# Optimization experiments

Measured on AMD Instinct MI355X. Metric: run time of the kernel, lower is better.

Reference implementation:

```python
import jax, jax.numpy as jnp
import numpy as np

NUM_HEADS = 12

def setup_inputs() -> dict:
    key = jax.random.key(0)
    k1, k2, k3 = jax.random.split(key, 3)
    B, N, C = 8, 2048, 768
    x = jax.random.normal(k1, (B, N, C), dtype=jnp.float32)
    w_qkv = jax.random.normal(k2, (3 * C, C), dtype=jnp.float32) * (C ** -0.5)
    w_proj = jax.random.normal(k3, (C, C), dtype=jnp.float32) * (C ** -0.5)
    b_proj = jnp.zeros((C,), dtype=jnp.float32)
    return {"x": x, "w_qkv": w_qkv, "w_proj": w_proj, "b_proj": b_proj}

def reference(x, w_qkv, w_proj, b_proj):
    B, N, C = x.shape
    H = NUM_HEADS
    D = C // H
    scale = D ** -0.5
    # qkv: [B,N,3C] -> [3,B,H,N,D]
    qkv = (x @ w_qkv.T).reshape(B, N, 3, H, D).transpose(2, 0, 3, 1, 4)
    q, k, v = qkv[0], qkv[1], qkv[2]
    attn = jnp.einsum('bhnd,bhmd->bhnm', q, k) * scale  # [B,H,N,N]
    attn = jax.nn.softmax(attn, axis=-1)
    out = jnp.einsum('bhnm,bhmd->bhnd', attn, v)  # [B,H,N,D]
    out = out.transpose(0, 2, 1, 3).reshape(B, N, C)
    return out @ w_proj.T + b_proj
```

## Files before the change

kernel.cpp:

```cpp
#include <hip/hip_runtime.h>

typedef __bf16 bf16;
typedef __attribute__((ext_vector_type(8))) __bf16 bf16x8;
typedef __attribute__((ext_vector_type(4))) __bf16 bf16x4;
typedef __attribute__((ext_vector_type(4))) float f32x4;

#define NBATCH 8
#define NHEAD  12
#define SEQ    2048
#define DH     64
#define CDIM   768
#define MROWS  (NBATCH*SEQ)
#define NQKV   (3*CDIM)

__device__ __forceinline__ f32x4 mfma16(bf16x8 a, bf16x8 b, f32x4 c) {
  return __builtin_amdgcn_mfma_f32_16x16x32_bf16(a, b, c, 0, 0, 0);
}

__device__ __forceinline__ void gload_lds16(const void* g, void* l) {
  __builtin_amdgcn_global_load_lds((const __attribute__((address_space(1))) void*)g,
                                   (__attribute__((address_space(3))) void*)l,
                                   16, 0, 0);
}

__device__ __forceinline__ unsigned cvt_pk_bf16(float lo, float hi) {
  unsigned r;
  asm("v_cvt_pk_bf16_f32 %0, %1, %2" : "=v"(r) : "v"(lo), "v"(hi));
  return r;
}

__device__ __forceinline__ float exp2_raw(float x) {
  float r;
  asm("v_exp_f32 %0, %1" : "=v"(r) : "v"(x));
  return r;
}

__global__ void cvt_bf16(const float* __restrict__ src, bf16* __restrict__ dst, int n8) {
  int i = blockIdx.x * 256 + threadIdx.x;
  if (i >= n8) return;
  const float4* s4 = (const float4*)src;
  float4 a = s4[2*i], c = s4[2*i+1];
  bf16x8 o;
  o[0]=(bf16)a.x; o[1]=(bf16)a.y; o[2]=(bf16)a.z; o[3]=(bf16)a.w;
  o[4]=(bf16)c.x; o[5]=(bf16)c.y; o[6]=(bf16)c.z; o[7]=(bf16)c.w;
  *(bf16x8*)(dst + (size_t)i*8) = o;
}

template <int OUT_F32>
__global__ __launch_bounds__(256, 2)
void gemm_bt(const bf16* __restrict__ A, const bf16* __restrict__ Bm,
             void* __restrict__ Cout, const float* __restrict__ bias,
             int M, int Nn, int K) {
  __shared__ bf16 As[128*32];
  __shared__ bf16 Bs[128*32];
  const int tid = threadIdx.x, wid = tid >> 6, lane = tid & 63;
  const int g = lane >> 4, ln = lane & 15;
  const int ntn = Nn >> 7;
  const int gsz = 32 * ntn;
  const int grp = blockIdx.x / gsz;
  const int rem = blockIdx.x - grp * gsz;
  const int tm = grp * 32 + (rem & 31);
  const int tn = rem >> 5;
  const int m0 = tm << 7, n0 = tn << 7;
  const int wr = wid >> 1, wc = wid & 1;

  const int srow = lane >> 2;
  const int sslot = lane & 3;

  f32x4 acc[4][4] = {};

  const int nkt = K >> 5;
  for (int kt = 0; kt < nkt; ++kt) {
    if (kt) __syncthreads();
    #pragma unroll
    for (int i = 0; i < 2; ++i) {
      int c = wid * 2 + i;
      int row = c * 16 + srow;
      int colA = kt * 32 + ((sslot ^ (row & 3)) << 3);
      gload_lds16(A + (size_t)(m0 + row) * K + colA, &As[c * 512]);
      gload_lds16(Bm + (size_t)(n0 + row) * K + colA, &Bs[c * 512]);
    }
    __syncthreads();

    bf16x8 aF[4], bF[4];
    #pragma unroll
    for (int m = 0; m < 4; ++m) {
      int row = wr * 64 + m * 16 + ln;
      aF[m] = *(const bf16x8*)&As[row * 32 + ((g ^ (row & 3)) << 3)];
    }
    #pragma unroll
    for (int n = 0; n < 4; ++n) {
      int row = wc * 64 + n * 16 + ln;
      bF[n] = *(const bf16x8*)&Bs[row * 32 + ((g ^ (row & 3)) << 3)];
    }
    #pragma unroll
    for (int m = 0; m < 4; ++m)
      #pragma unroll
      for (int n = 0; n < 4; ++n)
        acc[m][n] = mfma16(aF[m], bF[n], acc[m][n]);
  }

  #pragma unroll
  for (int m = 0; m < 4; ++m) {
    int rowb = m0 + wr * 64 + m * 16 + g * 4;
    #pragma unroll
    for (int n = 0; n < 4; ++n) {
      int col = n0 + wc * 64 + n * 16 + ln;
      float bv = OUT_F32 ? bias[col] : 0.f;
      #pragma unroll
      for (int r = 0; r < 4; ++r) {
        if (OUT_F32)
          ((float*)Cout)[(size_t)(rowb + r) * Nn + col] = acc[m][n][r] + bv;
        else
          ((bf16*)Cout)[(size_t)(rowb + r) * Nn + col] = (bf16)acc[m][n][r];
      }
    }
  }
}

__global__ __launch_bounds__(256)
void split_v(const bf16* __restrict__ qkv, bf16* __restrict__ Vt) {
  __shared__ bf16 vlds[64 * 72];
  const int nt = blockIdx.x, bh = blockIdx.y;
  const int b = bh / NHEAD, h = bh % NHEAD;
  const int tid = threadIdx.x;
  const int nl = tid >> 2, quad = tid & 3;

  const bf16* s = qkv + ((size_t)(b * SEQ + nt * 64 + nl)) * NQKV + 2 * CDIM + h * DH + quad * 16;
  *(bf16x8*)&vlds[nl * 72 + quad * 16] = *(const bf16x8*)s;
  *(bf16x8*)&vlds[nl * 72 + quad * 16 + 8] = *(const bf16x8*)(s + 8);
  __syncthreads();
  const int dl = tid >> 2;
  bf16x8 w0, w1;
  #pragma unroll
  for (int j = 0; j < 8; ++j) {
    w0[j] = vlds[(quad * 16 + j) * 72 + dl];
    w1[j] = vlds[(quad * 16 + 8 + j) * 72 + dl];
  }
  bf16* d = Vt + ((size_t)bh * DH + dl) * SEQ + nt * 64 + quad * 16;
  *(bf16x8*)d = w0;
  *(bf16x8*)(d + 8) = w1;
}

__global__ __launch_bounds__(128, 2)
void attn_fwd8(const bf16* __restrict__ qkv, const bf16* __restrict__ Vt,
               bf16* __restrict__ Oa) {
  __shared__ bf16 Ks[2][64 * 64];
  __shared__ bf16 Vs[2][64 * 64];
  const int tid = threadIdx.x, wid = tid >> 6, lane = tid & 63;
  const int g = lane >> 4, ln = lane & 15;
  const int qt = blockIdx.x, bh = blockIdx.y;
  const int b = bh / NHEAD, h = bh % NHEAD;

  const bf16* QrowA = qkv + ((size_t)b * SEQ + qt * 64 + wid * 32 + ln) * NQKV + h * DH;
  const bf16* QrowB = QrowA + (size_t)16 * NQKV;
  const bf16x8 qA0 = *(const bf16x8*)(QrowA + g * 8);
  const bf16x8 qA1 = *(const bf16x8*)(QrowA + 32 + g * 8);
  const bf16x8 qB0 = *(const bf16x8*)(QrowB + g * 8);
  const bf16x8 qB1 = *(const bf16x8*)(QrowB + 32 + g * 8);

  const int sr = lane >> 3, sl = lane & 7;
  const bf16* kp[4];
  const bf16* vp[4];
  int lofs[4];
  #pragma unroll
  for (int i = 0; i < 4; ++i) {
    const int c = wid * 4 + i;
    const int pr = c * 8 + sr;
    const int sw = (sl ^ (pr & 7)) << 3;
    const int keyK = ((pr >> 5) & 1) * 32 + ((pr >> 4) & 1) * 4 + ((pr >> 2) & 3) * 8 + (pr & 3);
    kp[i] = qkv + ((size_t)b * SEQ + keyK) * NQKV + CDIM + h * DH + sw;
    vp[i] = Vt + ((size_t)bh * DH + pr) * SEQ + sw;
    lofs[i] = c * 512;
  }
  const size_t KADV = (size_t)64 * NQKV;

  const int e7 = ln & 7;
  const int off0 = ln * 64 + ((g ^ e7) << 3);
  const int off1 = ln * 64 + (((4 | g) ^ e7) << 3);

  const bf16 one = (bf16)1.0f;
  const bf16x8 onesF = {one, one, one, one, one, one, one, one};

  f32x4 oA[4] = {}, oB[4] = {};
  f32x4 laccA = {0.f, 0.f, 0.f, 0.f}, laccB = {0.f, 0.f, 0.f, 0.f};
  float mA = -3.0e38f, mB = -3.0e38f;
  const float SC = 0.125f * 1.44269504088896f;

  #pragma unroll
  for (int i = 0; i < 4; ++i) {
    gload_lds16(kp[i], &Ks[0][lofs[i]]);
    gload_lds16(vp[i], &Vs[0][lofs[i]]);
  }
  __syncthreads();

  int cur = 0;
  for (int t = 0; t < SEQ / 64; ++t) {
    if (t < SEQ / 64 - 1) {
      const int nb = cur ^ 1;
      #pragma unroll
      for (int i = 0; i < 4; ++i) {
        kp[i] += KADV; vp[i] += 64;
        gload_lds16(kp[i], &Ks[nb][lofs[i]]);
        gload_lds16(vp[i], &Vs[nb][lofs[i]]);
      }
    }
    const bf16* KsB = &Ks[cur][0];
    const bf16* VsB = &Vs[cur][0];

    f32x4 sA[4] = {}, sB[4] = {};
    #pragma unroll
    for (int nt = 0; nt < 4; ++nt) {
      bf16x8 kF0 = *(const bf16x8*)(KsB + off0 + nt * 1024);
      bf16x8 kF1 = *(const bf16x8*)(KsB + off1 + nt * 1024);
      sA[nt] = mfma16(kF0, qA0, sA[nt]);
      sA[nt] = mfma16(kF1, qA1, sA[nt]);
      sB[nt] = mfma16(kF0, qB0, sB[nt]);
      sB[nt] = mfma16(kF1, qB1, sB[nt]);
    }

    float a0 = fmaxf(fmaxf(sA[0][0], sA[0][1]), fmaxf(sA[0][2], sA[0][3]));
    float a1 = fmaxf(fmaxf(sA[1][0], sA[1][1]), fmaxf(sA[1][2], sA[1][3]));
    float a2 = fmaxf(fmaxf(sA[2][0], sA[2][1]), fmaxf(sA[2][2], sA[2][3]));
    float a3 = fmaxf(fmaxf(sA[3][0], sA[3][1]), fmaxf(sA[3][2], sA[3][3]));
    float rA = fmaxf(fmaxf(a0, a1), fmaxf(a2, a3));
    rA = fmaxf(rA, __shfl_xor(rA, 16, 64));
    rA = fmaxf(rA, __shfl_xor(rA, 32, 64));
    float b0 = fmaxf(fmaxf(sB[0][0], sB[0][1]), fmaxf(sB[0][2], sB[0][3]));
    float b1 = fmaxf(fmaxf(sB[1][0], sB[1][1]), fmaxf(sB[1][2], sB[1][3]));
    float b2 = fmaxf(fmaxf(sB[2][0], sB[2][1]), fmaxf(sB[2][2], sB[2][3]));
    float b3 = fmaxf(fmaxf(sB[3][0], sB[3][1]), fmaxf(sB[3][2], sB[3][3]));
    float rB = fmaxf(fmaxf(b0, b1), fmaxf(b2, b3));
    rB = fmaxf(rB, __shfl_xor(rB, 16, 64));
    rB = fmaxf(rB, __shfl_xor(rB, 32, 64));
    const float rsA = rA * SC, rsB = rB * SC;

    if (__any(rsA > mA + 8.0f || rsB > mB + 8.0f)) {
      float nmA = fmaxf(mA, rsA), nmB = fmaxf(mB, rsB);
      float alA = exp2_raw(mA - nmA), alB = exp2_raw(mB - nmB);
      mA = nmA; mB = nmB;
      float alrA[4], alrB[4];
      #pragma unroll
      for (int r = 0; r < 4; ++r) {
        alrA[r] = __shfl(alA, g * 4 + r, 64);
        alrB[r] = __shfl(alB, g * 4 + r, 64);
      }
      #pragma unroll
      for (int dt = 0; dt < 4; ++dt)
        #pragma unroll
        for (int r = 0; r < 4; ++r) { oA[dt][r] *= alrA[r]; oB[dt][r] *= alrB[r]; }
      #pragma unroll
      for (int r = 0; r < 4; ++r) { laccA[r] *= alrA[r]; laccB[r] *= alrB[r]; }
    }

    bf16x8 pA[2], pB[2];
    #pragma unroll
    for (int kk = 0; kk < 2; ++kk) {
      union { bf16x8 v; unsigned u[4]; } w;
      w.u[0] = cvt_pk_bf16(exp2_raw(fmaf(sA[2*kk][0], SC, -mA)),
                           exp2_raw(fmaf(sA[2*kk][1], SC, -mA)));
      w.u[1] = cvt_pk_bf16(exp2_raw(fmaf(sA[2*kk][2], SC, -mA)),
                           exp2_raw(fmaf(sA[2*kk][3], SC, -mA)));
      w.u[2] = cvt_pk_bf16(exp2_raw(fmaf(sA[2*kk+1][0], SC, -mA)),
                           exp2_raw(fmaf(sA[2*kk+1][1], SC, -mA)));
      w.u[3] = cvt_pk_bf16(exp2_raw(fmaf(sA[2*kk+1][2], SC, -mA)),
                           exp2_raw(fmaf(sA[2*kk+1][3], SC, -mA)));
      pA[kk] = w.v;
      w.u[0] = cvt_pk_bf16(exp2_raw(fmaf(sB[2*kk][0], SC, -mB)),
                           exp2_raw(fmaf(sB[2*kk][1], SC, -mB)));
      w.u[1] = cvt_pk_bf16(exp2_raw(fmaf(sB[2*kk][2], SC, -mB)),
                           exp2_raw(fmaf(sB[2*kk][3], SC, -mB)));
      w.u[2] = cvt_pk_bf16(exp2_raw(fmaf(sB[2*kk+1][0], SC, -mB)),
                           exp2_raw(fmaf(sB[2*kk+1][1], SC, -mB)));
      w.u[3] = cvt_pk_bf16(exp2_raw(fmaf(sB[2*kk+1][2], SC, -mB)),
                           exp2_raw(fmaf(sB[2*kk+1][3], SC, -mB)));
      pB[kk] = w.v;
    }

    #pragma unroll
    for (int kk = 0; kk < 2; ++kk) {
      laccA = mfma16(pA[kk], onesF, laccA);
      laccB = mfma16(pB[kk], onesF, laccB);
      const int voff = kk ? off1 : off0;
      #pragma unroll
      for (int dt = 0; dt < 4; ++dt) {
        bf16x8 vF = *(const bf16x8*)(VsB + voff + dt * 1024);
        oA[dt] = mfma16(pA[kk], vF, oA[dt]);
        oB[dt] = mfma16(pB[kk], vF, oB[dt]);
      }
    }
    __syncthreads();
    cur ^= 1;
  }

  float invA[4], invB[4];
  #pragma unroll
  for (int r = 0; r < 4; ++r) { invA[r] = 1.0f / laccA[r]; invB[r] = 1.0f / laccB[r]; }

  #pragma unroll
  for (int r = 0; r < 4; ++r) {
    bf16* OrA = Oa + ((size_t)b * SEQ + qt * 64 + wid * 32 + g * 4 + r) * CDIM + h * DH + ln;
    bf16* OrB = OrA + (size_t)16 * CDIM;
    #pragma unroll
    for (int dt = 0; dt < 4; ++dt) {
      OrA[dt * 16] = (bf16)(oA[dt][r] * invA[r]);
      OrB[dt * 16] = (bf16)(oB[dt][r] * invB[r]);
    }
  }
}

extern "C" void kernel_launch(void* const* d_in, const int* in_sizes, int n_in,
                              void* d_out, int out_size, void* d_ws, size_t ws_size,
                              hipStream_t stream) {
  const float* x      = (const float*)d_in[0];
  const float* w_qkv  = (const float*)d_in[1];
  const float* w_proj = (const float*)d_in[2];
  const float* b_proj = (const float*)d_in[3];

  char* ws = (char*)d_ws;
  bf16* x_bf    = (bf16*)(ws + 0);
  bf16* wqkv_bf = (bf16*)(ws + 25165824);
  bf16* wproj_bf= (bf16*)(ws + 28704768);
  bf16* qkv     = (bf16*)(ws + 29884416);
  bf16* attn_o  = (bf16*)(ws + 105381888);
  bf16* Vtb     = (bf16*)(ws + 130547712);

  cvt_bf16<<<dim3((MROWS*CDIM/8 + 255)/256), 256, 0, stream>>>(x, x_bf, MROWS*CDIM/8);
  cvt_bf16<<<dim3((NQKV*CDIM/8 + 255)/256), 256, 0, stream>>>(w_qkv, wqkv_bf, NQKV*CDIM/8);
  cvt_bf16<<<dim3((CDIM*CDIM/8 + 255)/256), 256, 0, stream>>>(w_proj, wproj_bf, CDIM*CDIM/8);

  gemm_bt<0><<<dim3((MROWS/128)*(NQKV/128)), 256, 0, stream>>>(
      x_bf, wqkv_bf, qkv, nullptr, MROWS, NQKV, CDIM);

  split_v<<<dim3(SEQ/64, NBATCH*NHEAD), 256, 0, stream>>>(qkv, Vtb);

  attn_fwd8<<<dim3(SEQ/64, NBATCH*NHEAD), 128, 0, stream>>>(qkv, Vtb, attn_o);

  gemm_bt<1><<<dim3((MROWS/128)*(CDIM/128)), 256, 0, stream>>>(
      attn_o, wproj_bf, (float*)d_out, b_proj, MROWS, CDIM, CDIM);
}
```

Before: 311.9 us.

## Triple-buffer K/V loads and overlap next-tile QK^T with current softmax

The attention kernel moves from double to triple buffering of K/V tiles in LDS, with explicit vmcnt waits replacing full barriers so two tiles stay in flight. It also software-pipelines the loop by computing the QK^T scores for the next tile while the current tile's softmax and PV run, using two ping-pong score register sets. s_setprio raises wave priority around the MFMA section. The aim is to hide global-load and softmax latency behind matrix work, at the cost of more LDS and registers, which may reduce occupancy under launch_bounds(128,2).

```diff
diff --git a/kernel.cpp b/kernel.cpp
--- a/kernel.cpp
+++ b/kernel.cpp
@@ -143,10 +143,10 @@
 }
 
 __global__ __launch_bounds__(128, 2)
-void attn_fwd8(const bf16* __restrict__ qkv, const bf16* __restrict__ Vt,
-               bf16* __restrict__ Oa) {
-  __shared__ bf16 Ks[2][64 * 64];
-  __shared__ bf16 Vs[2][64 * 64];
+void attn_fwd10(const bf16* __restrict__ qkv, const bf16* __restrict__ Vt,
+                bf16* __restrict__ Oa) {
+  __shared__ bf16 Ks[3 * 4096];
+  __shared__ bf16 Vs[3 * 4096];
   const int tid = threadIdx.x, wid = tid >> 6, lane = tid & 63;
   const int g = lane >> 4, ln = lane & 15;
   const int qt = blockIdx.x, bh = blockIdx.y;
@@ -187,111 +187,140 @@
   float mA = -3.0e38f, mB = -3.0e38f;
   const float SC = 0.125f * 1.44269504088896f;
 
-  #pragma unroll
-  for (int i = 0; i < 4; ++i) {
-    gload_lds16(kp[i], &Ks[0][lofs[i]]);
-    gload_lds16(vp[i], &Vs[0][lofs[i]]);
-  }
-  __syncthreads();
-
-  int cur = 0;
-  for (int t = 0; t < SEQ / 64; ++t) {
-    if (t < SEQ / 64 - 1) {
-      const int nb = cur ^ 1;
-      #pragma unroll
-      for (int i = 0; i < 4; ++i) {
-        kp[i] += KADV; vp[i] += 64;
-        gload_lds16(kp[i], &Ks[nb][lofs[i]]);
-        gload_lds16(vp[i], &Vs[nb][lofs[i]]);
-      }
-    }
-    const bf16* KsB = &Ks[cur][0];
-    const bf16* VsB = &Vs[cur][0];
-
-    f32x4 sA[4] = {}, sB[4] = {};
-    #pragma unroll
-    for (int nt = 0; nt < 4; ++nt) {
-      bf16x8 kF0 = *(const bf16x8*)(KsB + off0 + nt * 1024);
-      bf16x8 kF1 = *(const bf16x8*)(KsB + off1 + nt * 1024);
-      sA[nt] = mfma16(kF0, qA0, sA[nt]);
-      sA[nt] = mfma16(kF1, qA1, sA[nt]);
-      sB[nt] = mfma16(kF0, qB0, sB[nt]);
-      sB[nt] = mfma16(kF1, qB1, sB[nt]);
-    }
-
-    float a0 = fmaxf(fmaxf(sA[0][0], sA[0][1]), fmaxf(sA[0][2], sA[0][3]));
-    float a1 = fmaxf(fmaxf(sA[1][0], sA[1][1]), fmaxf(sA[1][2], sA[1][3]));
-    float a2 = fmaxf(fmaxf(sA[2][0], sA[2][1]), fmaxf(sA[2][2], sA[2][3]));
-    float a3 = fmaxf(fmaxf(sA[3][0], sA[3][1]), fmaxf(sA[3][2], sA[3][3]));
-    float rA = fmaxf(fmaxf(a0, a1), fmaxf(a2, a3));
-    rA = fmaxf(rA, __shfl_xor(rA, 16, 64));
-    rA = fmaxf(rA, __shfl_xor(rA, 32, 64));
-    float b0 = fmaxf(fmaxf(sB[0][0], sB[0][1]), fmaxf(sB[0][2], sB[0][3]));
-    float b1 = fmaxf(fmaxf(sB[1][0], sB[1][1]), fmaxf(sB[1][2], sB[1][3]));
-    float b2 = fmaxf(fmaxf(sB[2][0], sB[2][1]), fmaxf(sB[2][2], sB[2][3]));
-    float b3 = fmaxf(fmaxf(sB[3][0], sB[3][1]), fmaxf(sB[3][2], sB[3][3]));
-    float rB = fmaxf(fmaxf(b0, b1), fmaxf(b2, b3));
-    rB = fmaxf(rB, __shfl_xor(rB, 16, 64));
-    rB = fmaxf(rB, __shfl_xor(rB, 32, 64));
-    const float rsA = rA * SC, rsB = rB * SC;
-
-    if (__any(rsA > mA + 8.0f || rsB > mB + 8.0f)) {
-      float nmA = fmaxf(mA, rsA), nmB = fmaxf(mB, rsB);
-      float alA = exp2_raw(mA - nmA), alB = exp2_raw(mB - nmB);
-      mA = nmA; mB = nmB;
-      float alrA[4], alrB[4];
-      #pragma unroll
-      for (int r = 0; r < 4; ++r) {
-        alrA[r] = __shfl(alA, g * 4 + r, 64);
-        alrB[r] = __shfl(alB, g * 4 + r, 64);
-      }
-      #pragma unroll
-      for (int dt = 0; dt < 4; ++dt)
-        #pragma unroll
-        for (int r = 0; r < 4; ++r) { oA[dt][r] *= alrA[r]; oB[dt][r] *= alrB[r]; }
-      #pragma unroll
-      for (int r = 0; r < 4; ++r) { laccA[r] *= alrA[r]; laccB[r] *= alrB[r]; }
-    }
-
-    bf16x8 pA[2], pB[2];
-    #pragma unroll
-    for (int kk = 0; kk < 2; ++kk) {
-      union { bf16x8 v; unsigned u[4]; } w;
-      w.u[0] = cvt_pk_bf16(exp2_raw(fmaf(sA[2*kk][0], SC, -mA)),
-                           exp2_raw(fmaf(sA[2*kk][1], SC, -mA)));
-      w.u[1] = cvt_pk_bf16(exp2_raw(fmaf(sA[2*kk][2], SC, -mA)),
-                           exp2_raw(fmaf(sA[2*kk][3], SC, -mA)));
-      w.u[2] = cvt_pk_bf16(exp2_raw(fmaf(sA[2*kk+1][0], SC, -mA)),
-                           exp2_raw(fmaf(sA[2*kk+1][1], SC, -mA)));
-      w.u[3] = cvt_pk_bf16(exp2_raw(fmaf(sA[2*kk+1][2], SC, -mA)),
-                           exp2_raw(fmaf(sA[2*kk+1][3], SC, -mA)));
-      pA[kk] = w.v;
-      w.u[0] = cvt_pk_bf16(exp2_raw(fmaf(sB[2*kk][0], SC, -mB)),
-                           exp2_raw(fmaf(sB[2*kk][1], SC, -mB)));
-      w.u[1] = cvt_pk_bf16(exp2_raw(fmaf(sB[2*kk][2], SC, -mB)),
-                           exp2_raw(fmaf(sB[2*kk][3], SC, -mB)));
-      w.u[2] = cvt_pk_bf16(exp2_raw(fmaf(sB[2*kk+1][0], SC, -mB)),
-                           exp2_raw(fmaf(sB[2*kk+1][1], SC, -mB)));
-      w.u[3] = cvt_pk_bf16(exp2_raw(fmaf(sB[2*kk+1][2], SC, -mB)),
-                           exp2_raw(fmaf(sB[2*kk+1][3], SC, -mB)));
-      pB[kk] = w.v;
-    }
-
-    #pragma unroll
-    for (int kk = 0; kk < 2; ++kk) {
-      laccA = mfma16(pA[kk], onesF, laccA);
-      laccB = mfma16(pB[kk], onesF, laccB);
-      const int voff = kk ? off1 : off0;
-      #pragma unroll
-      for (int dt = 0; dt < 4; ++dt) {
-        bf16x8 vF = *(const bf16x8*)(VsB + voff + dt * 1024);
-        oA[dt] = mfma16(pA[kk], vF, oA[dt]);
-        oB[dt] = mfma16(pB[kk], vF, oB[dt]);
-      }
-    }
-    __syncthreads();
-    cur ^= 1;
-  }
+  f32x4 sA0[4] = {}, sB0[4] = {}, sA1[4] = {}, sB1[4] = {};
+
+#define STAGE(DST) do {                                           \
+    _Pragma("unroll")                                             \
+    for (int i = 0; i < 4; ++i) {                                 \
+      gload_lds16(kp[i], &Ks[(DST) + lofs[i]]);                   \
+      gload_lds16(vp[i], &Vs[(DST) + lofs[i]]);                   \
+      kp[i] += KADV; vp[i] += 64;                                 \
+    }                                                             \
+  } while (0)
+
+#define QKT(KOFS, SA, SB) do {                                    \
+    const bf16* KsB_ = &Ks[(KOFS)];                               \
+    _Pragma("unroll")                                             \
+    for (int nt = 0; nt < 4; ++nt) {                              \
+      bf16x8 kF0 = *(const bf16x8*)(KsB_ + off0 + nt * 1024);     \
+      bf16x8 kF1 = *(const bf16x8*)(KsB_ + off1 + nt * 1024);     \
+      SA[nt] = mfma16(kF0, qA0, SA[nt]);                          \
+      SA[nt] = mfma16(kF1, qA1, SA[nt]);                          \
+      SB[nt] = mfma16(kF0, qB0, SB[nt]);                          \
+      SB[nt] = mfma16(kF1, qB1, SB[nt]);                          \
+    }                                                             \
+  } while (0)
+
+  STAGE(0);
+  STAGE(4096);
+  STAGE(8192);
+  asm volatile("s_waitcnt vmcnt(16)" ::: "memory");
+  __builtin_amdgcn_s_barrier();
+  __builtin_amdgcn_sched_barrier(0);
+  QKT(0, sA0, sB0);
+
+  const int NT = SEQ / 64;
+  int cur = 0, nxt = 4096, stg = 8192;
+
+#define ITER(T, SC_A, SC_B, SN_A, SN_B) do {                                  \
+    if ((T) < NT - 2) asm volatile("s_waitcnt vmcnt(8)" ::: "memory");        \
+    else              asm volatile("s_waitcnt vmcnt(0)" ::: "memory");        \
+    __builtin_amdgcn_s_barrier();                                             \
+    __builtin_amdgcn_sched_barrier(0);                                        \
+                                \
+    float a0 = fmaxf(fmaxf(SC_A[0][0], SC_A[0][1]), fmaxf(SC_A[0][2], SC_A[0][3])); \
+    float a1 = fmaxf(fmaxf(SC_A[1][0], SC_A[1][1]), fmaxf(SC_A[1][2], SC_A[1][3])); \
+    float a2 = fmaxf(fmaxf(SC_A[2][0], SC_A[2][1]), fmaxf(SC_A[2][2], SC_A[2][3])); \
+    float a3 = fmaxf(fmaxf(SC_A[3][0], SC_A[3][1]), fmaxf(SC_A[3][2], SC_A[3][3])); \
+    float rA = fmaxf(fmaxf(a0, a1), fmaxf(a2, a3));                           \
+    rA = fmaxf(rA, __shfl_xor(rA, 16, 64));                                   \
+    rA = fmaxf(rA, __shfl_xor(rA, 32, 64));                                   \
+    float b0_ = fmaxf(fmaxf(SC_B[0][0], SC_B[0][1]), fmaxf(SC_B[0][2], SC_B[0][3])); \
+    float b1_ = fmaxf(fmaxf(SC_B[1][0], SC_B[1][1]), fmaxf(SC_B[1][2], SC_B[1][3])); \
+    float b2_ = fmaxf(fmaxf(SC_B[2][0], SC_B[2][1]), fmaxf(SC_B[2][2], SC_B[2][3])); \
+    float b3_ = fmaxf(fmaxf(SC_B[3][0], SC_B[3][1]), fmaxf(SC_B[3][2], SC_B[3][3])); \
+    float rB = fmaxf(fmaxf(b0_, b1_), fmaxf(b2_, b3_));                       \
+    rB = fmaxf(rB, __shfl_xor(rB, 16, 64));                                   \
+    rB = fmaxf(rB, __shfl_xor(rB, 32, 64));                                   \
+    const float rsA = rA * SC, rsB = rB * SC;                                 \
+    __builtin_amdgcn_s_setprio(1);                                            \
+      \
+    if ((T) < NT - 1) { QKT(nxt, SN_A, SN_B); }                               \
+                                                         \
+    if (__any(rsA > mA + 8.0f || rsB > mB + 8.0f)) {                          \
+      float nmA = fmaxf(mA, rsA), nmB = fmaxf(mB, rsB);                       \
+      float alA = exp2_raw(mA - nmA), alB = exp2_raw(mB - nmB);               \
+      mA = nmA; mB = nmB;                                                     \
+      float alrA[4], alrB[4];                                                 \
+      _Pragma("unroll")                                                       \
+      for (int r = 0; r < 4; ++r) {                                           \
+        alrA[r] = __shfl(alA, g * 4 + r, 64);                                 \
+        alrB[r] = __shfl(alB, g * 4 + r, 64);                                 \
+      }                                                                       \
+      _Pragma("unroll")                                                       \
+      for (int dt = 0; dt < 4; ++dt)                                          \
+        _Pragma("unroll")                                                     \
+        for (int r = 0; r < 4; ++r) { oA[dt][r] *= alrA[r]; oB[dt][r] *= alrB[r]; } \
+      _Pragma("unroll")                                                       \
+      for (int r = 0; r < 4; ++r) { laccA[r] *= alrA[r]; laccB[r] *= alrB[r]; } \
+    }                                                                         \
+                 \
+    bf16x8 pA[2], pB[2];                                                      \
+    _Pragma("unroll")                                                         \
+    for (int kk = 0; kk < 2; ++kk) {                                          \
+      union { bf16x8 v; unsigned u[4]; } w;                                   \
+      w.u[0] = cvt_pk_bf16(exp2_raw(fmaf(SC_A[2*kk][0], SC, -mA)),            \
+                           exp2_raw(fmaf(SC_A[2*kk][1], SC, -mA)));           \
+      w.u[1] = cvt_pk_bf16(exp2_raw(fmaf(SC_A[2*kk][2], SC, -mA)),            \
+                           exp2_raw(fmaf(SC_A[2*kk][3], SC, -mA)));           \
+      w.u[2] = cvt_pk_bf16(exp2_raw(fmaf(SC_A[2*kk+1][0], SC, -mA)),          \
+                           exp2_raw(fmaf(SC_A[2*kk+1][1], SC, -mA)));         \
+      w.u[3] = cvt_pk_bf16(exp2_raw(fmaf(SC_A[2*kk+1][2], SC, -mA)),          \
+                           exp2_raw(fmaf(SC_A[2*kk+1][3], SC, -mA)));         \
+      pA[kk] = w.v;                                                           \
+      w.u[0] = cvt_pk_bf16(exp2_raw(fmaf(SC_B[2*kk][0], SC, -mB)),            \
+                           exp2_raw(fmaf(SC_B[2*kk][1], SC, -mB)));           \
+      w.u[1] = cvt_pk_bf16(exp2_raw(fmaf(SC_B[2*kk][2], SC, -mB)),            \
+                           exp2_raw(fmaf(SC_B[2*kk][3], SC, -mB)));           \
+      w.u[2] = cvt_pk_bf16(exp2_raw(fmaf(SC_B[2*kk+1][0], SC, -mB)),          \
+                           exp2_raw(fmaf(SC_B[2*kk+1][1], SC, -mB)));         \
+      w.u[3] = cvt_pk_bf16(exp2_raw(fmaf(SC_B[2*kk+1][2], SC, -mB)),          \
+                           exp2_raw(fmaf(SC_B[2*kk+1][3], SC, -mB)));         \
+      pB[kk] = w.v;                                                           \
+    }                                                                         \
+                   \
+    _Pragma("unroll")                                                         \
+    for (int nt = 0; nt < 4; ++nt) {                                          \
+      f32x4 z = {0.f, 0.f, 0.f, 0.f};                                         \
+      SC_A[nt] = z; SC_B[nt] = z;                                             \
+    }                                                                         \
+                                                \
+    _Pragma("unroll")                                                         \
+    for (int kk = 0; kk < 2; ++kk) {                                          \
+      laccA = mfma16(pA[kk], onesF, laccA);                                   \
+      laccB = mfma16(pB[kk], onesF, laccB);                                   \
+      const int voff = (kk ? off1 : off0) + cur;                              \
+      _Pragma("unroll")                                                       \
+      for (int dt = 0; dt < 4; ++dt) {                                        \
+        bf16x8 vF = *(const bf16x8*)(&Vs[0] + voff + dt * 1024);              \
+        oA[dt] = mfma16(pA[kk], vF, oA[dt]);                                  \
+        oB[dt] = mfma16(pB[kk], vF, oB[dt]);                                  \
+      }                                                                       \
+    }                                                                         \
+    __builtin_amdgcn_s_setprio(0);                                            \
+    __builtin_amdgcn_sched_barrier(0);                                        \
+    __builtin_amdgcn_s_barrier();                                             \
+    if ((T) + 3 < NT) { STAGE(cur); }                                         \
+    { int tmp = cur; cur = nxt; nxt = stg; stg = tmp; }                       \
+  } while (0)
+
+  for (int t = 0; t < NT; t += 2) {
+    ITER(t,     sA0, sB0, sA1, sB1);
+    ITER(t + 1, sA1, sB1, sA0, sB0);
+  }
+#undef ITER
+#undef QKT
+#undef STAGE
 
   float invA[4], invB[4];
   #pragma unroll
@@ -334,7 +363,7 @@
 
   split_v<<<dim3(SEQ/64, NBATCH*NHEAD), 256, 0, stream>>>(qkv, Vtb);
 
-  attn_fwd8<<<dim3(SEQ/64, NBATCH*NHEAD), 128, 0, stream>>>(qkv, Vtb, attn_o);
+  attn_fwd10<<<dim3(SEQ/64, NBATCH*NHEAD), 128, 0, stream>>>(qkv, Vtb, attn_o);
 
   gemm_bt<1><<<dim3((MROWS/128)*(CDIM/128)), 256, 0, stream>>>(
       attn_o, wproj_bf, (float*)d_out, b_proj, MROWS, CDIM, CDIM);
```

Result: slower. 318.5 us (+2.1%).
